# Kernel optimization log

Hardware: AMD Instinct MI355X
Metric: run time of the kernel (lower is better)

The kernel has to match this reference:

```python
import jax, jax.numpy as jnp
import numpy as np

B, H, HKV, S, D = 2, 32, 8, 2048, 64
SCALE = 0.125  # 1/sqrt(D)
EPS = 1e-9     # kernel divides by (l + 1e-9)


def setup_inputs() -> dict:
    key = jax.random.key(0)
    kq, kk, kv = jax.random.split(key, 3)
    Q = jax.random.normal(kq, (B, H, S, D), dtype=jnp.float32)
    K = jax.random.normal(kk, (B, HKV, S, D), dtype=jnp.float32)
    V = jax.random.normal(kv, (B, HKV, S, D), dtype=jnp.float32)
    return {"Q": Q, "K": K, "V": V}


def reference(Q, K, V):
    # Grouped-query attention with KV-head sharing, non-causal, full softmax.
    b, h, s, d = Q.shape
    hkv = K.shape[1]
    g = h // hkv  # query heads per kv head; h = kvh*g + gi (contiguous groups)
    Qg = Q.reshape(b, hkv, g, s, d)
    # scores: [b, hkv, g, s_q, s_k]
    scores = jnp.einsum("bkgsd,bktd->bkgst", Qg, K) * SCALE
    m = jnp.max(scores, axis=-1, keepdims=True)
    p = jnp.exp(scores - m)
    l = jnp.sum(p, axis=-1, keepdims=True)  # [b,hkv,g,s,1]
    out = jnp.einsum("bkgst,bktd->bkgsd", p, V) / (l + EPS)
    return out.reshape(b, h, s, d)
```

## Files before the change

kernel.cpp:

```cpp
#include <hip/hip_runtime.h>

#define NB 2
#define NH 32
#define NKV 8
#define SEQ 2048
#define DH 64
#define TQ 256
#define TK 64
#define KPAD 8

typedef _Float16 f16x4 __attribute__((ext_vector_type(4)));
typedef _Float16 f16x8 __attribute__((ext_vector_type(8)));
typedef float f32x4 __attribute__((ext_vector_type(4)));

#define MFMA(A, B, C) __builtin_amdgcn_mfma_f32_16x16x32_f16(A, B, C, 0, 0, 0)

__global__ __launch_bounds__(256, 2) void gqa_fused(
    const float* __restrict__ Qg, const float* __restrict__ Kg,
    const float* __restrict__ Vg, float* __restrict__ Og) {
  __shared__ _Float16 Kt[TK][DH + KPAD];
  __shared__ _Float16 Vt[DH][TK + KPAD];
  __shared__ _Float16 Pt[TQ][TK + KPAD];

  const int tid  = threadIdx.x;
  const int wave = tid >> 6;
  const int lane = tid & 63;
  const int quad = lane >> 4;
  const int l16  = lane & 15;

  const int qt  = blockIdx.x;
  const int hq  = blockIdx.y;
  const int b   = blockIdx.z;
  const int hkv = hq >> 2;

  const float* Qb = Qg + (((size_t)b * NH + hq) * SEQ + (size_t)qt * TQ) * DH;
  const float* Kb = Kg + ((size_t)b * NKV + hkv) * (size_t)SEQ * DH;
  const float* Vb = Vg + ((size_t)b * NKV + hkv) * (size_t)SEQ * DH;
  float* Ob       = Og + (((size_t)b * NH + hq) * SEQ + (size_t)qt * TQ) * DH;

  const float qscale = 0.125f * 1.44269504088896341f;

  f16x8 aQ[4][2];
#pragma unroll
  for (int sl = 0; sl < 4; ++sl) {
    const float* qp = Qb + (size_t)(wave * 64 + sl * 16 + l16) * DH + quad * 8;
#pragma unroll
    for (int c = 0; c < 2; ++c) {
      const float4 f0 = *reinterpret_cast<const float4*>(qp + c * 32);
      const float4 f1 = *reinterpret_cast<const float4*>(qp + c * 32 + 4);
      union { f16x8 v; _Float16 e[8]; } u;
      u.e[0] = (_Float16)(f0.x * qscale);
      u.e[1] = (_Float16)(f0.y * qscale);
      u.e[2] = (_Float16)(f0.z * qscale);
      u.e[3] = (_Float16)(f0.w * qscale);
      u.e[4] = (_Float16)(f1.x * qscale);
      u.e[5] = (_Float16)(f1.y * qscale);
      u.e[6] = (_Float16)(f1.z * qscale);
      u.e[7] = (_Float16)(f1.w * qscale);
      aQ[sl][c] = u.v;
    }
  }

  f32x4 o[4][4], ol[4];
#pragma unroll
  for (int sl = 0; sl < 4; ++sl) {
    ol[sl] = (f32x4){0.f, 0.f, 0.f, 0.f};
#pragma unroll
    for (int n = 0; n < 4; ++n) o[sl][n] = (f32x4){0.f, 0.f, 0.f, 0.f};
  }
  const f16x8 ones = {(_Float16)1.f, (_Float16)1.f, (_Float16)1.f, (_Float16)1.f,
                      (_Float16)1.f, (_Float16)1.f, (_Float16)1.f, (_Float16)1.f};

  const int kkey = tid >> 3;
  const int kd8  = (tid & 7) << 3;
  float4 kpre[2][2];
  float vpre[2][8];
  auto load_tile = [&](int kt) {
#pragma unroll
    for (int it = 0; it < 2; ++it) {
      const float* kp = Kb + (size_t)(kt + it * 32 + kkey) * DH + kd8;
      kpre[it][0] = *reinterpret_cast<const float4*>(kp);
      kpre[it][1] = *reinterpret_cast<const float4*>(kp + 4);
    }
#pragma unroll
    for (int ao = 0; ao < 2; ++ao) {
      const int a = wave + 4 * ao;
      const float* vp = Vb + (size_t)(kt + 2 * a) * DH + lane;
#pragma unroll
      for (int t = 0; t < 4; ++t) {
        vpre[ao][t]     = vp[(size_t)(16 * t) * DH];
        vpre[ao][t + 4] = vp[(size_t)(16 * t + 1) * DH];
      }
    }
  };

  load_tile(0);

  for (int kt = 0; kt < SEQ; kt += TK) {
    __syncthreads();

#pragma unroll
    for (int it = 0; it < 2; ++it) {
      union { f16x8 v; _Float16 e[8]; } u;
      u.e[0] = (_Float16)kpre[it][0].x;
      u.e[1] = (_Float16)kpre[it][0].y;
      u.e[2] = (_Float16)kpre[it][0].z;
      u.e[3] = (_Float16)kpre[it][0].w;
      u.e[4] = (_Float16)kpre[it][1].x;
      u.e[5] = (_Float16)kpre[it][1].y;
      u.e[6] = (_Float16)kpre[it][1].z;
      u.e[7] = (_Float16)kpre[it][1].w;
      *reinterpret_cast<f16x8*>(&Kt[it * 32 + kkey][kd8]) = u.v;
    }
#pragma unroll
    for (int ao = 0; ao < 2; ++ao) {
      union { f16x8 v; _Float16 e[8]; } u;
#pragma unroll
      for (int j = 0; j < 8; ++j) u.e[j] = (_Float16)vpre[ao][j];
      *reinterpret_cast<f16x8*>(&Vt[lane][8 * (wave + 4 * ao)]) = u.v;
    }
    __syncthreads();

    if (kt + TK < SEQ) load_tile(kt + TK);

    f16x8 bK[4][2];
#pragma unroll
    for (int n = 0; n < 4; ++n)
#pragma unroll
      for (int c = 0; c < 2; ++c)
        bK[n][c] =
            *reinterpret_cast<const f16x8*>(&Kt[n * 16 + l16][c * 32 + quad * 8]);

    f32x4 s[4][4];
#pragma unroll
    for (int sl = 0; sl < 4; ++sl)
#pragma unroll
      for (int n = 0; n < 4; ++n) {
        f32x4 acc = (f32x4){0.f, 0.f, 0.f, 0.f};
        acc = MFMA(aQ[sl][0], bK[n][0], acc);
        acc = MFMA(aQ[sl][1], bK[n][1], acc);
        s[sl][n] = acc;
      }

#pragma unroll
    for (int sl = 0; sl < 4; ++sl) {
      const int prow = wave * 64 + sl * 16 + quad * 4;
#pragma unroll
      for (int r = 0; r < 4; ++r) {
        union { f16x4 v; _Float16 e[4]; } u;
#pragma unroll
        for (int n = 0; n < 4; ++n)
          u.e[n] = (_Float16)__builtin_amdgcn_exp2f(s[sl][n][r]);
        *reinterpret_cast<f16x4*>(&Pt[prow + r][4 * l16]) = u.v;
      }
    }
    __asm__ volatile("s_waitcnt lgkmcnt(0)" ::: "memory");

    f16x8 aP[4][2], bV[4][2];
#pragma unroll
    for (int sl = 0; sl < 4; ++sl)
#pragma unroll
      for (int c = 0; c < 2; ++c)
        aP[sl][c] = *reinterpret_cast<const f16x8*>(
            &Pt[wave * 64 + sl * 16 + l16][c * 32 + quad * 8]);
#pragma unroll
    for (int n = 0; n < 4; ++n)
#pragma unroll
      for (int c = 0; c < 2; ++c)
        bV[n][c] =
            *reinterpret_cast<const f16x8*>(&Vt[n * 16 + l16][c * 32 + quad * 8]);

#pragma unroll
    for (int sl = 0; sl < 4; ++sl) {
      ol[sl] = MFMA(aP[sl][0], ones, ol[sl]);
      ol[sl] = MFMA(aP[sl][1], ones, ol[sl]);
#pragma unroll
      for (int n = 0; n < 4; ++n) {
        o[sl][n] = MFMA(aP[sl][0], bV[n][0], o[sl][n]);
        o[sl][n] = MFMA(aP[sl][1], bV[n][1], o[sl][n]);
      }
    }
  }

#pragma unroll
  for (int sl = 0; sl < 4; ++sl)
#pragma unroll
    for (int r = 0; r < 4; ++r) {
      const float inv = 1.f / (ol[sl][r] + 1e-9f);
      const size_t row = (size_t)(wave * 64 + sl * 16 + quad * 4 + r);
#pragma unroll
      for (int n = 0; n < 4; ++n)
        Ob[row * DH + n * 16 + l16] = o[sl][n][r] * inv;
    }
}

extern "C" void kernel_launch(void* const* d_in, const int* in_sizes, int n_in,
                              void* d_out, int out_size, void* d_ws, size_t ws_size,
                              hipStream_t stream) {
  const float* Q = (const float*)d_in[0];
  const float* K = (const float*)d_in[1];
  const float* V = (const float*)d_in[2];
  float* O = (float*)d_out;
  dim3 grid(SEQ / TQ, NH, NB);
  gqa_fused<<<grid, 256, 0, stream>>>(Q, K, V, O);
}
```

Measured before the change: 162.7 us.

## Use 512-thread blocks with 32 query rows per wave and XOR-swizzled LDS

Doubles the block to 8 waves so each wave owns 32 query rows instead of 64. This halves the per-wave accumulator and score registers, and each thread loads half as much of the K/V tile. The padded shared-memory arrays are replaced by an XOR-swizzled layout to avoid bank conflicts without padding, and the score computation is interleaved per slice with the exp and P store. The aim is higher occupancy and less register pressure, at the cost of more waves contending for the barriers and the same LDS traffic for the K/V fragments spread over more waves.

```diff
diff --git a/kernel.cpp b/kernel.cpp
--- a/kernel.cpp
+++ b/kernel.cpp
@@ -7,7 +7,6 @@
 #define DH 64
 #define TQ 256
 #define TK 64
-#define KPAD 8
 
 typedef _Float16 f16x4 __attribute__((ext_vector_type(4)));
 typedef _Float16 f16x8 __attribute__((ext_vector_type(8)));
@@ -15,12 +14,16 @@
 
 #define MFMA(A, B, C) __builtin_amdgcn_mfma_f32_16x16x32_f16(A, B, C, 0, 0, 0)
 
-__global__ __launch_bounds__(256, 2) void gqa_fused(
+__device__ __forceinline__ int swz(int row, int hcol) {
+  return (row << 6) + ((((hcol >> 3) ^ (row & 7)) << 3) | (hcol & 7));
+}
+
+__global__ __launch_bounds__(512, 4) void gqa_fused(
     const float* __restrict__ Qg, const float* __restrict__ Kg,
     const float* __restrict__ Vg, float* __restrict__ Og) {
-  __shared__ _Float16 Kt[TK][DH + KPAD];
-  __shared__ _Float16 Vt[DH][TK + KPAD];
-  __shared__ _Float16 Pt[TQ][TK + KPAD];
+  __shared__ _Float16 Kt[TK * DH];
+  __shared__ _Float16 Vt[DH * TK];
+  __shared__ _Float16 Pt[TQ * TK];
 
   const int tid  = threadIdx.x;
   const int wave = tid >> 6;
@@ -40,10 +43,10 @@
 
   const float qscale = 0.125f * 1.44269504088896341f;
 
-  f16x8 aQ[4][2];
+  f16x8 aQ[2][2];
 #pragma unroll
-  for (int sl = 0; sl < 4; ++sl) {
-    const float* qp = Qb + (size_t)(wave * 64 + sl * 16 + l16) * DH + quad * 8;
+  for (int sl = 0; sl < 2; ++sl) {
+    const float* qp = Qb + (size_t)(wave * 32 + sl * 16 + l16) * DH + quad * 8;
 #pragma unroll
     for (int c = 0; c < 2; ++c) {
       const float4 f0 = *reinterpret_cast<const float4*>(qp + c * 32);
@@ -61,9 +64,9 @@
     }
   }
 
-  f32x4 o[4][4], ol[4];
+  f32x4 o[2][4], ol[2];
 #pragma unroll
-  for (int sl = 0; sl < 4; ++sl) {
+  for (int sl = 0; sl < 2; ++sl) {
     ol[sl] = (f32x4){0.f, 0.f, 0.f, 0.f};
 #pragma unroll
     for (int n = 0; n < 4; ++n) o[sl][n] = (f32x4){0.f, 0.f, 0.f, 0.f};
@@ -73,24 +76,17 @@
 
   const int kkey = tid >> 3;
   const int kd8  = (tid & 7) << 3;
-  float4 kpre[2][2];
-  float vpre[2][8];
+  float4 kpre[2];
+  float vpre[8];
   auto load_tile = [&](int kt) {
+    const float* kp = Kb + (size_t)(kt + kkey) * DH + kd8;
+    kpre[0] = *reinterpret_cast<const float4*>(kp);
+    kpre[1] = *reinterpret_cast<const float4*>(kp + 4);
+    const float* vp = Vb + (size_t)(kt + 2 * wave) * DH + lane;
 #pragma unroll
-    for (int it = 0; it < 2; ++it) {
-      const float* kp = Kb + (size_t)(kt + it * 32 + kkey) * DH + kd8;
-      kpre[it][0] = *reinterpret_cast<const float4*>(kp);
-      kpre[it][1] = *reinterpret_cast<const float4*>(kp + 4);
-    }
-#pragma unroll
-    for (int ao = 0; ao < 2; ++ao) {
-      const int a = wave + 4 * ao;
-      const float* vp = Vb + (size_t)(kt + 2 * a) * DH + lane;
-#pragma unroll
-      for (int t = 0; t < 4; ++t) {
-        vpre[ao][t]     = vp[(size_t)(16 * t) * DH];
-        vpre[ao][t + 4] = vp[(size_t)(16 * t + 1) * DH];
-      }
+    for (int t = 0; t < 4; ++t) {
+      vpre[t]     = vp[(size_t)(16 * t) * DH];
+      vpre[t + 4] = vp[(size_t)(16 * t + 1) * DH];
     }
   };
 
@@ -99,25 +95,23 @@
   for (int kt = 0; kt < SEQ; kt += TK) {
     __syncthreads();
 
-#pragma unroll
-    for (int it = 0; it < 2; ++it) {
+    {
       union { f16x8 v; _Float16 e[8]; } u;
-      u.e[0] = (_Float16)kpre[it][0].x;
-      u.e[1] = (_Float16)kpre[it][0].y;
-      u.e[2] = (_Float16)kpre[it][0].z;
-      u.e[3] = (_Float16)kpre[it][0].w;
-      u.e[4] = (_Float16)kpre[it][1].x;
-      u.e[5] = (_Float16)kpre[it][1].y;
-      u.e[6] = (_Float16)kpre[it][1].z;
-      u.e[7] = (_Float16)kpre[it][1].w;
-      *reinterpret_cast<f16x8*>(&Kt[it * 32 + kkey][kd8]) = u.v;
+      u.e[0] = (_Float16)kpre[0].x;
+      u.e[1] = (_Float16)kpre[0].y;
+      u.e[2] = (_Float16)kpre[0].z;
+      u.e[3] = (_Float16)kpre[0].w;
+      u.e[4] = (_Float16)kpre[1].x;
+      u.e[5] = (_Float16)kpre[1].y;
+      u.e[6] = (_Float16)kpre[1].z;
+      u.e[7] = (_Float16)kpre[1].w;
+      *reinterpret_cast<f16x8*>(&Kt[swz(kkey, kd8)]) = u.v;
     }
-#pragma unroll
-    for (int ao = 0; ao < 2; ++ao) {
+    {
       union { f16x8 v; _Float16 e[8]; } u;
 #pragma unroll
-      for (int j = 0; j < 8; ++j) u.e[j] = (_Float16)vpre[ao][j];
-      *reinterpret_cast<f16x8*>(&Vt[lane][8 * (wave + 4 * ao)]) = u.v;
+      for (int j = 0; j < 8; ++j) u.e[j] = (_Float16)vpre[j];
+      *reinterpret_cast<f16x8*>(&Vt[swz(lane, wave << 3)]) = u.v;
     }
     __syncthreads();
 
@@ -128,50 +122,47 @@
     for (int n = 0; n < 4; ++n)
 #pragma unroll
       for (int c = 0; c < 2; ++c)
-        bK[n][c] =
-            *reinterpret_cast<const f16x8*>(&Kt[n * 16 + l16][c * 32 + quad * 8]);
+        bK[n][c] = *reinterpret_cast<const f16x8*>(
+            &Kt[swz(n * 16 + l16, c * 32 + quad * 8)]);
 
-    f32x4 s[4][4];
 #pragma unroll
-    for (int sl = 0; sl < 4; ++sl)
+    for (int sl = 0; sl < 2; ++sl) {
+      f32x4 s[4];
 #pragma unroll
       for (int n = 0; n < 4; ++n) {
         f32x4 acc = (f32x4){0.f, 0.f, 0.f, 0.f};
         acc = MFMA(aQ[sl][0], bK[n][0], acc);
         acc = MFMA(aQ[sl][1], bK[n][1], acc);
-        s[sl][n] = acc;
+        s[n] = acc;
       }
-
-#pragma unroll
-    for (int sl = 0; sl < 4; ++sl) {
-      const int prow = wave * 64 + sl * 16 + quad * 4;
+      const int prow = wave * 32 + sl * 16 + quad * 4;
 #pragma unroll
       for (int r = 0; r < 4; ++r) {
         union { f16x4 v; _Float16 e[4]; } u;
 #pragma unroll
         for (int n = 0; n < 4; ++n)
-          u.e[n] = (_Float16)__builtin_amdgcn_exp2f(s[sl][n][r]);
-        *reinterpret_cast<f16x4*>(&Pt[prow + r][4 * l16]) = u.v;
+          u.e[n] = (_Float16)__builtin_amdgcn_exp2f(s[n][r]);
+        *reinterpret_cast<f16x4*>(&Pt[swz(prow + r, l16 << 2)]) = u.v;
       }
     }
     __asm__ volatile("s_waitcnt lgkmcnt(0)" ::: "memory");
 
-    f16x8 aP[4][2], bV[4][2];
+    f16x8 aP[2][2], bV[4][2];
 #pragma unroll
-    for (int sl = 0; sl < 4; ++sl)
+    for (int sl = 0; sl < 2; ++sl)
 #pragma unroll
       for (int c = 0; c < 2; ++c)
         aP[sl][c] = *reinterpret_cast<const f16x8*>(
-            &Pt[wave * 64 + sl * 16 + l16][c * 32 + quad * 8]);
+            &Pt[swz(wave * 32 + sl * 16 + l16, c * 32 + quad * 8)]);
 #pragma unroll
     for (int n = 0; n < 4; ++n)
 #pragma unroll
       for (int c = 0; c < 2; ++c)
-        bV[n][c] =
-            *reinterpret_cast<const f16x8*>(&Vt[n * 16 + l16][c * 32 + quad * 8]);
+        bV[n][c] = *reinterpret_cast<const f16x8*>(
+            &Vt[swz(n * 16 + l16, c * 32 + quad * 8)]);
 
 #pragma unroll
-    for (int sl = 0; sl < 4; ++sl) {
+    for (int sl = 0; sl < 2; ++sl) {
       ol[sl] = MFMA(aP[sl][0], ones, ol[sl]);
       ol[sl] = MFMA(aP[sl][1], ones, ol[sl]);
 #pragma unroll
@@ -183,11 +174,11 @@
   }
 
 #pragma unroll
-  for (int sl = 0; sl < 4; ++sl)
+  for (int sl = 0; sl < 2; ++sl)
 #pragma unroll
     for (int r = 0; r < 4; ++r) {
       const float inv = 1.f / (ol[sl][r] + 1e-9f);
-      const size_t row = (size_t)(wave * 64 + sl * 16 + quad * 4 + r);
+      const size_t row = (size_t)(wave * 32 + sl * 16 + quad * 4 + r);
 #pragma unroll
       for (int n = 0; n < 4; ++n)
         Ob[row * DH + n * 16 + l16] = o[sl][n][r] * inv;
@@ -202,5 +193,5 @@
   const float* V = (const float*)d_in[2];
   float* O = (float*)d_out;
   dim3 grid(SEQ / TQ, NH, NB);
-  gqa_fused<<<grid, 256, 0, stream>>>(Q, K, V, O);
+  gqa_fused<<<grid, 512, 0, stream>>>(Q, K, V, O);
 }
```

After: 189.7 us. 16.6% more time.

## Double-buffer K/V shared tiles with XOR-swizzled LDS layout, one barrier per step

Applied to the files above, without the earlier changes.

Replaces the padded LDS arrays with XOR-swizzled unpadded layouts for K, V and P, and double-buffers the K and V tiles. The next tile is written into the alternate buffer after the MFMA work, so each iteration needs one barrier instead of two. The aim is to cut barrier stalls and LDS bank conflicts. LDS use grows from the second K/V buffer, which may reduce occupancy. The per-wave P buffer stays single and relies on the end-of-iteration barrier.

```diff
diff --git a/kernel.cpp b/kernel.cpp
--- a/kernel.cpp
+++ b/kernel.cpp
@@ -7,7 +7,6 @@
 #define DH 64
 #define TQ 256
 #define TK 64
-#define KPAD 8
 
 typedef _Float16 f16x4 __attribute__((ext_vector_type(4)));
 typedef _Float16 f16x8 __attribute__((ext_vector_type(8)));
@@ -15,12 +14,16 @@
 
 #define MFMA(A, B, C) __builtin_amdgcn_mfma_f32_16x16x32_f16(A, B, C, 0, 0, 0)
 
+__device__ __forceinline__ int swz(int row, int hcol) {
+  return (row << 6) + ((((hcol >> 3) ^ (row & 7)) << 3) | (hcol & 7));
+}
+
 __global__ __launch_bounds__(256, 2) void gqa_fused(
     const float* __restrict__ Qg, const float* __restrict__ Kg,
     const float* __restrict__ Vg, float* __restrict__ Og) {
-  __shared__ _Float16 Kt[TK][DH + KPAD];
-  __shared__ _Float16 Vt[DH][TK + KPAD];
-  __shared__ _Float16 Pt[TQ][TK + KPAD];
+  __shared__ _Float16 Kt[2][TK * DH];
+  __shared__ _Float16 Vt[2][DH * TK];
+  __shared__ _Float16 Pt[TQ * TK];
 
   const int tid  = threadIdx.x;
   const int wave = tid >> 6;
@@ -94,11 +97,7 @@
     }
   };
 
-  load_tile(0);
-
-  for (int kt = 0; kt < SEQ; kt += TK) {
-    __syncthreads();
-
+  auto stage_tile = [&](int buf) {
 #pragma unroll
     for (int it = 0; it < 2; ++it) {
       union { f16x8 v; _Float16 e[8]; } u;
@@ -110,26 +109,33 @@
       u.e[5] = (_Float16)kpre[it][1].y;
       u.e[6] = (_Float16)kpre[it][1].z;
       u.e[7] = (_Float16)kpre[it][1].w;
-      *reinterpret_cast<f16x8*>(&Kt[it * 32 + kkey][kd8]) = u.v;
+      *reinterpret_cast<f16x8*>(&Kt[buf][swz(it * 32 + kkey, kd8)]) = u.v;
     }
 #pragma unroll
     for (int ao = 0; ao < 2; ++ao) {
       union { f16x8 v; _Float16 e[8]; } u;
 #pragma unroll
       for (int j = 0; j < 8; ++j) u.e[j] = (_Float16)vpre[ao][j];
-      *reinterpret_cast<f16x8*>(&Vt[lane][8 * (wave + 4 * ao)]) = u.v;
-    }
-    __syncthreads();
-
-    if (kt + TK < SEQ) load_tile(kt + TK);
+      *reinterpret_cast<f16x8*>(&Vt[buf][swz(lane, 8 * (wave + 4 * ao))]) = u.v;
+    }
+  };
+
+  load_tile(0);
+  stage_tile(0);
+  __syncthreads();
+
+  for (int kt = 0; kt < SEQ; kt += TK) {
+    const int cur  = (kt >> 6) & 1;
+    const bool more = (kt + TK) < SEQ;
+    if (more) load_tile(kt + TK);
 
     f16x8 bK[4][2];
 #pragma unroll
     for (int n = 0; n < 4; ++n)
 #pragma unroll
       for (int c = 0; c < 2; ++c)
-        bK[n][c] =
-            *reinterpret_cast<const f16x8*>(&Kt[n * 16 + l16][c * 32 + quad * 8]);
+        bK[n][c] = *reinterpret_cast<const f16x8*>(
+            &Kt[cur][swz(n * 16 + l16, c * 32 + quad * 8)]);
 
     f32x4 s[4][4];
 #pragma unroll
@@ -151,7 +157,7 @@
 #pragma unroll
         for (int n = 0; n < 4; ++n)
           u.e[n] = (_Float16)__builtin_amdgcn_exp2f(s[sl][n][r]);
-        *reinterpret_cast<f16x4*>(&Pt[prow + r][4 * l16]) = u.v;
+        *reinterpret_cast<f16x4*>(&Pt[swz(prow + r, l16 << 2)]) = u.v;
       }
     }
     __asm__ volatile("s_waitcnt lgkmcnt(0)" ::: "memory");
@@ -162,13 +168,13 @@
 #pragma unroll
       for (int c = 0; c < 2; ++c)
         aP[sl][c] = *reinterpret_cast<const f16x8*>(
-            &Pt[wave * 64 + sl * 16 + l16][c * 32 + quad * 8]);
+            &Pt[swz(wave * 64 + sl * 16 + l16, c * 32 + quad * 8)]);
 #pragma unroll
     for (int n = 0; n < 4; ++n)
 #pragma unroll
       for (int c = 0; c < 2; ++c)
-        bV[n][c] =
-            *reinterpret_cast<const f16x8*>(&Vt[n * 16 + l16][c * 32 + quad * 8]);
+        bV[n][c] = *reinterpret_cast<const f16x8*>(
+            &Vt[cur][swz(n * 16 + l16, c * 32 + quad * 8)]);
 
 #pragma unroll
     for (int sl = 0; sl < 4; ++sl) {
@@ -180,6 +186,9 @@
         o[sl][n] = MFMA(aP[sl][1], bV[n][1], o[sl][n]);
       }
     }
+
+    if (more) stage_tile(cur ^ 1);
+    __syncthreads();
   }
 
 #pragma unroll
```

After: 169.3 us. 4.1% more time.
